# Kernel optimization log

Measured on AMD Instinct MI355X. Metric: run time of the kernel, lower is better.

The kernel has to match this reference:

```python
import jax, jax.numpy as jnp
import numpy as np

N_NODES = 100000
N_EDGES = 1600000
IN_CH, HID_CH, OUT_CH = 128, 128, 64


def _spmm(row, col, val, x, n):
    # COO sparse @ dense: out[r] += val_e * x[col_e]
    gathered = val[:, None] * x[col]  # [E, d]
    return jax.ops.segment_sum(gathered, row, num_segments=n)


def setup_inputs() -> dict:
    key = jax.random.key(0)
    ks = jax.random.split(key, 8)
    x = jax.random.normal(ks[0], (N_NODES, IN_CH), dtype=jnp.float32)
    adj_row = jax.random.randint(ks[1], (N_EDGES,), 0, N_NODES)
    adj_col = jax.random.randint(ks[2], (N_EDGES,), 0, N_NODES)
    adj_val = jax.random.uniform(ks[3], (N_EDGES,), dtype=jnp.float32)
    w1 = jax.random.normal(ks[4], (IN_CH, HID_CH), dtype=jnp.float32) * (1.0 / np.sqrt(IN_CH))
    b1 = jax.random.normal(ks[5], (HID_CH,), dtype=jnp.float32) * 0.01
    w2 = jax.random.normal(ks[6], (HID_CH, OUT_CH), dtype=jnp.float32) * (1.0 / np.sqrt(HID_CH))
    b2 = jax.random.normal(ks[7], (OUT_CH,), dtype=jnp.float32) * 0.01
    return {"x": x, "adj_row": adj_row, "adj_col": adj_col, "adj_val": adj_val,
            "w1": w1, "b1": b1, "w2": w2, "b2": b2}


def reference(x, adj_row, adj_col, adj_val, w1, b1, w2, b2):
    n = x.shape[0]
    # layer 1: spmm -> linear -> relu
    h = _spmm(adj_row, adj_col, adj_val, x, n)
    h = jax.nn.relu(h @ w1 + b1)
    # layer 2: spmm -> linear
    h = _spmm(adj_row, adj_col, adj_val, h, n)
    return h @ w2 + b2
```

## Files before the change

### kernel.cpp

```cpp
#include <hip/hip_runtime.h>


typedef __bf16 v8bf __attribute__((ext_vector_type(8)));
typedef float  v4f  __attribute__((ext_vector_type(4)));

#define MAXB 800

__device__ __forceinline__ unsigned short f2bf(float f) {
    unsigned u = __float_as_uint(f);
    unsigned r = u + 0x7fffu + ((u >> 16) & 1u);
    return (unsigned short)(r >> 16);
}

__global__ __launch_bounds__(256) void prep_k(const float* __restrict__ w1,
                                              const float* __restrict__ w2,
                                              unsigned short* __restrict__ w1T,
                                              unsigned short* __restrict__ w2T,
                                              int* __restrict__ counts,
                                              int* __restrict__ rowptr,
                                              int2* __restrict__ epkS, int E, int N) {
    int i = blockIdx.x * 256 + threadIdx.x;
    if (i < 16384) {
        int n = i >> 7, k = i & 127;
        w1T[i] = f2bf(w1[k * 128 + n]);
    } else if (i < 24576) {
        int i2 = i - 16384;
        int n = i2 >> 7, k = i2 & 127;
        w2T[i2] = f2bf(w2[k * 64 + n]);
    } else if (i < 24576 + MAXB) {
        counts[i - 24576] = 0;
    } else if (i < 24576 + MAXB + 32) {
        epkS[E + (i - 24576 - MAXB)] = make_int2(0, 0);
    } else if (i == 24576 + MAXB + 32) {
        rowptr[N] = E;
    }
}

__global__ __launch_bounds__(256) void hist_b(const int* __restrict__ arow,
                                              int* __restrict__ counts, int E, int B) {
    __shared__ int lh[MAXB];
    const int tid = threadIdx.x;
    for (int i = tid; i < B; i += 256) lh[i] = 0;
    __syncthreads();
    const int base = blockIdx.x * 4096;
#pragma unroll
    for (int j = 0; j < 16; ++j) {
        int i = base + j * 256 + tid;
        if (i < E) atomicAdd(&lh[arow[i] >> 7], 1);
    }
    __syncthreads();
    for (int i = tid; i < B; i += 256) {
        int c = lh[i];
        if (c) atomicAdd(&counts[i], c);
    }
}

__global__ __launch_bounds__(256) void scan_s(const int* __restrict__ counts,
                                              int* __restrict__ boff,
                                              int* __restrict__ gcursor, int B, int E) {
    __shared__ int lds[256];
    const int t = threadIdx.x;
    const int b0 = t * 4;
    int v[4];
    int s = 0;
#pragma unroll
    for (int j = 0; j < 4; ++j) {
        v[j] = (b0 + j < B) ? counts[b0 + j] : 0;
        s += v[j];
    }
    lds[t] = s;
    __syncthreads();
    for (int off = 1; off < 256; off <<= 1) {
        int tmp = 0;
        if (t >= off) tmp = lds[t - off];
        __syncthreads();
        if (t >= off) lds[t] += tmp;
        __syncthreads();
    }
    int run = (t > 0) ? lds[t - 1] : 0;
#pragma unroll
    for (int j = 0; j < 4; ++j) {
        if (b0 + j < B) {
            boff[b0 + j] = run;
            gcursor[b0 + j] = run;
        }
        run += v[j];
    }
    if (t == 255) boff[B] = E;
}

__global__ __launch_bounds__(256) void partition_k(const int* __restrict__ arow,
                                                   const int* __restrict__ acol,
                                                   const float* __restrict__ aval,
                                                   int* __restrict__ gcursor,
                                                   int2* __restrict__ epk, int E, int B) {
    __shared__ int2 ldata[4096];
    __shared__ int ldest[4096];
    __shared__ int lhist[MAXB];
    __shared__ int lscan[MAXB];
    __shared__ int ldelta[MAXB];
    __shared__ int lcur[MAXB];
    __shared__ int stmp[256];
    const int tid = threadIdx.x;
    const int base = blockIdx.x * 4096;
    const int cnt = min(4096, E - base);

    for (int i = tid; i < MAXB; i += 256) {
        lhist[i] = 0;
        lcur[i] = 0;
    }
    __syncthreads();

    int rr[16];
#pragma unroll
    for (int j = 0; j < 16; ++j) {
        int i = base + j * 256 + tid;
        rr[j] = (i < E) ? arow[i] : -1;
        if (rr[j] >= 0) atomicAdd(&lhist[rr[j] >> 7], 1);
    }
    __syncthreads();

    const int b0 = tid * 4;
    int v[4];
    int s = 0;
#pragma unroll
    for (int j = 0; j < 4; ++j) {
        v[j] = (b0 + j < MAXB) ? lhist[b0 + j] : 0;
        s += v[j];
    }
    stmp[tid] = s;
    __syncthreads();
    for (int off = 1; off < 256; off <<= 1) {
        int tmp = 0;
        if (tid >= off) tmp = stmp[tid - off];
        __syncthreads();
        if (tid >= off) stmp[tid] += tmp;
        __syncthreads();
    }
    int run = (tid > 0) ? stmp[tid - 1] : 0;
#pragma unroll
    for (int j = 0; j < 4; ++j) {
        if (b0 + j < MAXB) lscan[b0 + j] = run;
        run += v[j];
    }
    __syncthreads();

    for (int b = tid; b < B; b += 256) {
        int c = lhist[b];
        if (c) ldelta[b] = atomicAdd(&gcursor[b], c) - lscan[b];
    }
    __syncthreads();

#pragma unroll
    for (int j = 0; j < 16; ++j) {
        int i = base + j * 256 + tid;
        if (i < E) {
            int r = rr[j];
            int b = r >> 7;
            int lp = atomicAdd(&lcur[b], 1);
            int slot = lscan[b] + lp;
            int pk = acol[i] | ((r & 127) << 17);
            ldata[slot] = make_int2(pk, __float_as_int(aval[i]));
            ldest[slot] = ldelta[b] + slot;
        }
    }
    __syncthreads();

    for (int s2 = tid; s2 < cnt; s2 += 256) epk[ldest[s2]] = ldata[s2];
}

template <int NC, bool AF32>
__device__ __forceinline__ void gemm_body(const void* __restrict__ A,
                                          const unsigned short* __restrict__ wT,
                                          unsigned short* __restrict__ y, int M,
                                          int bid, char* smem) {
    constexpr int KP = 136;
    constexpr int NT = NC / 16;
    unsigned short* wl = (unsigned short*)smem;
    const int tid = threadIdx.x;
    for (int idx = tid; idx < NC * 16; idx += 256) {
        int n = idx >> 4, kc = idx & 15;
        *(uint4*)&wl[n * KP + kc * 8] = *(const uint4*)&wT[n * 128 + kc * 8];
    }
    __syncthreads();

    const int wave = tid >> 6;
    const int lane = tid & 63;
    const int m = lane & 15;
    const int q = lane >> 4;
    const int rowbase = bid * 64 + wave * 16;
    const int rowc = min(rowbase + m, M - 1);

    v4f acc[NT] = {};
    union LU { uint4 qv; v8bf b; };

#pragma unroll
    for (int ks = 0; ks < 4; ++ks) {
        const int k0 = ks * 32 + q * 8;
        v8bf a;
        if (AF32) {
            const float* Ap = (const float*)A + (size_t)rowc * 128 + k0;
            float4 f0 = *(const float4*)Ap;
            float4 f1 = *(const float4*)(Ap + 4);
            union { unsigned short s[8]; v8bf b; } cv;
            cv.s[0] = f2bf(f0.x); cv.s[1] = f2bf(f0.y);
            cv.s[2] = f2bf(f0.z); cv.s[3] = f2bf(f0.w);
            cv.s[4] = f2bf(f1.x); cv.s[5] = f2bf(f1.y);
            cv.s[6] = f2bf(f1.z); cv.s[7] = f2bf(f1.w);
            a = cv.b;
        } else {
            LU lu;
            lu.qv = *(const uint4*)((const unsigned short*)A + (size_t)rowc * 128 + k0);
            a = lu.b;
        }
#pragma unroll
        for (int nt = 0; nt < NT; ++nt) {
            v8bf b = *(const v8bf*)&wl[(nt * 16 + m) * KP + k0];
            acc[nt] = __builtin_amdgcn_mfma_f32_16x16x32_bf16(a, b, acc[nt], 0, 0, 0);
        }
    }
#pragma unroll
    for (int nt = 0; nt < NT; ++nt) {
#pragma unroll
        for (int r = 0; r < 4; ++r) {
            int orow = rowbase + q * 4 + r;
            if (orow < M) y[(size_t)orow * NC + nt * 16 + m] = f2bf(acc[nt][r]);
        }
    }
}

__global__ __launch_bounds__(256) void sort_gemm1(const int* __restrict__ boff,
                                                  const int2* __restrict__ epk,
                                                  int2* __restrict__ epkS,
                                                  int* __restrict__ rowptr, int N, int B,
                                                  const float* __restrict__ x,
                                                  const unsigned short* __restrict__ w1T,
                                                  unsigned short* __restrict__ y1b) {
    __shared__ __align__(16) char smem[34816];
    const int tid = threadIdx.x;
    if (blockIdx.x >= B) {
        gemm_body<128, true>(x, w1T, y1b, N, blockIdx.x - B, smem);
        return;
    }
    int2* sorted = (int2*)smem;
    int*  sc     = (int*)(smem + 32768);
    int*  lcur   = (int*)(smem + 32768 + 512);
    const int b = blockIdx.x;
    const int s = boff[b], e = boff[b + 1];
    const int cnt = min(e - s, 4096);
    if (tid < 128) sc[tid] = 0;
    __syncthreads();
    for (int i = s + tid; i < e; i += 256) {
        int rl = (epk[i].x >> 17) & 127;
        atomicAdd(&sc[rl], 1);
    }
    __syncthreads();
    int hv = (tid < 128) ? sc[tid] : 0;
    for (int off = 1; off < 128; off <<= 1) {
        int add = 0;
        if (tid < 128 && tid >= off) add = sc[tid - off];
        __syncthreads();
        if (tid < 128 && tid >= off) sc[tid] += add;
        __syncthreads();
    }
    if (tid < 128) {
        int ex = sc[tid] - hv;
        lcur[tid] = ex;
        int r = b * 128 + tid;
        if (r < N) rowptr[r] = s + ex;
    }
    __syncthreads();
    for (int i = s + tid; i < e; i += 256) {
        int2 p = epk[i];
        int rl = (p.x >> 17) & 127;
        int slot = atomicAdd(&lcur[rl], 1);
        if (slot < 4096) sorted[slot] = make_int2(p.x & 0x1FFFF, p.y);
    }
    __syncthreads();
    for (int i = tid; i < cnt; i += 256) epkS[s + i] = sorted[i];
}

__global__ __launch_bounds__(256) void gemm2_k(const unsigned short* __restrict__ h1b,
                                               const unsigned short* __restrict__ w2T,
                                               unsigned short* __restrict__ y2b, int M) {
    __shared__ __align__(16) char smem[64 * 136 * 2];
    gemm_body<64, false>(h1b, w2T, y2b, M, blockIdx.x, smem);
}

__global__ __launch_bounds__(256) void spmm128(const int* __restrict__ rowptr,
                                               const int2* __restrict__ ep,
                                               const unsigned short* __restrict__ yb,
                                               const float* __restrict__ bias,
                                               unsigned* __restrict__ outp, int N) {
    const int row = (blockIdx.x * 256 + threadIdx.x) >> 6;
    const int lane = threadIdx.x & 63;
    if (row >= N) return;
    const int s = rowptr[row], e = rowptr[row + 1];
    const unsigned* y32 = (const unsigned*)yb;
    float accx = 0.f, accy = 0.f;
    int2 cur[8];
#pragma unroll
    for (int k = 0; k < 8; ++k) cur[k] = ep[s + k];
    for (int j = s; j < e; j += 8) {
        int2 nxt[8];
#pragma unroll
        for (int k = 0; k < 8; ++k) nxt[k] = ep[j + 8 + k];
#pragma unroll
        for (int k = 0; k < 8; ++k) {
            float v = (j + k < e) ? __int_as_float(cur[k].y) : 0.f;
            unsigned u = y32[(size_t)cur[k].x * 64 + lane];
            accx += v * __uint_as_float(u << 16);
            accy += v * __uint_as_float(u & 0xffff0000u);
        }
#pragma unroll
        for (int k = 0; k < 8; ++k) cur[k] = nxt[k];
    }
    float2 bv = ((const float2*)bias)[lane];
    accx += bv.x;
    accy += bv.y;
    accx = fmaxf(accx, 0.f);
    accy = fmaxf(accy, 0.f);
    outp[(size_t)row * 64 + lane] = ((unsigned)f2bf(accy) << 16) | f2bf(accx);
}

__global__ __launch_bounds__(256) void spmm64(const int* __restrict__ rowptr,
                                              const int2* __restrict__ ep,
                                              const unsigned short* __restrict__ yb,
                                              const float* __restrict__ bias,
                                              float2* __restrict__ outp, int N) {
    const int row = (blockIdx.x * 256 + threadIdx.x) >> 6;
    const int lane = threadIdx.x & 63;
    if (row >= N) return;
    const int half = lane >> 5;
    const int sl = lane & 31;
    const int s = rowptr[row], e = rowptr[row + 1];
    const unsigned* y32 = (const unsigned*)yb;
    float accx = 0.f, accy = 0.f;
    int2 cur[8];
#pragma unroll
    for (int k = 0; k < 8; ++k) cur[k] = ep[s + 2 * k + half];
    for (int j = s; j < e; j += 16) {
        int2 nxt[8];
#pragma unroll
        for (int k = 0; k < 8; ++k) nxt[k] = ep[j + 16 + 2 * k + half];
#pragma unroll
        for (int k = 0; k < 8; ++k) {
            float v = (j + 2 * k + half < e) ? __int_as_float(cur[k].y) : 0.f;
            unsigned u = y32[(size_t)cur[k].x * 32 + sl];
            accx += v * __uint_as_float(u << 16);
            accy += v * __uint_as_float(u & 0xffff0000u);
        }
#pragma unroll
        for (int k = 0; k < 8; ++k) cur[k] = nxt[k];
    }
    accx += __shfl_xor(accx, 32, 64);
    accy += __shfl_xor(accy, 32, 64);
    if (sl == lane) {
        float2 bv = ((const float2*)bias)[sl];
        float2 o;
        o.x = accx + bv.x;
        o.y = accy + bv.y;
        outp[(size_t)row * 32 + sl] = o;
    }
}

extern "C" void kernel_launch(void* const* d_in, const int* in_sizes, int n_in,
                              void* d_out, int out_size, void* d_ws, size_t ws_size,
                              hipStream_t stream) {
    const float* x    = (const float*)d_in[0];
    const int*   arow = (const int*)d_in[1];
    const int*   acol = (const int*)d_in[2];
    const float* aval = (const float*)d_in[3];
    const float* w1   = (const float*)d_in[4];
    const float* b1   = (const float*)d_in[5];
    const float* w2   = (const float*)d_in[6];
    const float* b2   = (const float*)d_in[7];
    float*       out  = (float*)d_out;

    const int N = in_sizes[0] / 128;
    const int E = in_sizes[1];
    const int B = (N + 127) >> 7;

    char* p = (char*)d_ws;
    auto alloc = [&](size_t bytes) {
        char* r = p;
        p += (bytes + 255) & ~(size_t)255;
        return r;
    };
    int*            counts  = (int*)alloc((size_t)MAXB * 4);
    int*            boff    = (int*)alloc((size_t)(MAXB + 1) * 4);
    int*            gcursor = (int*)alloc((size_t)MAXB * 4);
    int*            rowptr  = (int*)alloc((size_t)(N + 1) * 4);
    int2*           epkS    = (int2*)alloc((size_t)(E + 32) * 8);
    unsigned short* w1T     = (unsigned short*)alloc(128 * 128 * 2);
    unsigned short* w2T     = (unsigned short*)alloc(64 * 128 * 2);
    unsigned short* y1b     = (unsigned short*)alloc((size_t)N * 128 * 2);
    unsigned short* h1b     = (unsigned short*)alloc((size_t)N * 128 * 2);
    unsigned short* y2b     = (unsigned short*)alloc((size_t)N * 64 * 2);
    int2*           epk     = (int2*)h1b;

    const int gemm_blocks = (N + 63) / 64;
    const int pb = (E + 4095) / 4096;

    prep_k<<<(24576 + MAXB + 33 + 255) / 256, 256, 0, stream>>>(
        w1, w2, w1T, w2T, counts, rowptr, epkS, E, N);
    hist_b<<<pb, 256, 0, stream>>>(arow, counts, E, B);
    scan_s<<<1, 256, 0, stream>>>(counts, boff, gcursor, B, E);
    partition_k<<<pb, 256, 0, stream>>>(arow, acol, aval, gcursor, epk, E, B);
    sort_gemm1<<<B + gemm_blocks, 256, 0, stream>>>(boff, epk, epkS, rowptr, N, B,
                                                    x, w1T, y1b);
    const int spmm_blocks = (N + 3) / 4;
    spmm128<<<spmm_blocks, 256, 0, stream>>>(rowptr, epkS, y1b, b1, (unsigned*)h1b, N);
    gemm2_k<<<gemm_blocks, 256, 0, stream>>>(h1b, w2T, y2b, N);
    spmm64<<<spmm_blocks, 256, 0, stream>>>(rowptr, epkS, y2b, b2, (float2*)out, N);
}
```

Before: 321.4 us.

## Fuse layer-1 SpMM with GEMM2 and merge weight prep into histogram

Layer-1 SpMM now writes each block's 64 rows of ReLU output into shared memory, and the same block immediately multiplies them by W2 with MFMA. This drops the h1 round trip through global memory and one launch. Weight conversion and padding are folded into the histogram kernel, and the counts buffer is zeroed with a memset. The final SpMM is rewritten so each lane handles one bf16 column with a 64-wide gather. Each wave now processes 16 rows serially in the fused kernel, which reduces parallelism and latency hiding for the gather. The edge-partition buffer now gets its own allocation instead of aliasing h1.

After: 313.7 us. -2.4%, faster.

```diff
diff --git a/kernel.cpp b/kernel.cpp
--- a/kernel.cpp
+++ b/kernel.cpp
@@ -12,34 +12,29 @@
     return (unsigned short)(r >> 16);
 }
 
-__global__ __launch_bounds__(256) void prep_k(const float* __restrict__ w1,
-                                              const float* __restrict__ w2,
-                                              unsigned short* __restrict__ w1T,
-                                              unsigned short* __restrict__ w2T,
-                                              int* __restrict__ counts,
-                                              int* __restrict__ rowptr,
-                                              int2* __restrict__ epkS, int E, int N) {
-    int i = blockIdx.x * 256 + threadIdx.x;
-    if (i < 16384) {
-        int n = i >> 7, k = i & 127;
-        w1T[i] = f2bf(w1[k * 128 + n]);
-    } else if (i < 24576) {
-        int i2 = i - 16384;
+__global__ __launch_bounds__(256) void hist_prep(const int* __restrict__ arow,
+                                                 int* __restrict__ counts, int E, int B,
+                                                 const float* __restrict__ w1,
+                                                 const float* __restrict__ w2,
+                                                 unsigned short* __restrict__ w1T,
+                                                 unsigned short* __restrict__ w2T,
+                                                 int* __restrict__ rowptr,
+                                                 int2* __restrict__ epkS, int N) {
+    const int tid = threadIdx.x;
+    int gi = blockIdx.x * 256 + tid;
+    if (gi < 16384) {
+        int n = gi >> 7, k = gi & 127;
+        w1T[gi] = f2bf(w1[k * 128 + n]);
+    } else if (gi < 24576) {
+        int i2 = gi - 16384;
         int n = i2 >> 7, k = i2 & 127;
         w2T[i2] = f2bf(w2[k * 64 + n]);
-    } else if (i < 24576 + MAXB) {
-        counts[i - 24576] = 0;
-    } else if (i < 24576 + MAXB + 32) {
-        epkS[E + (i - 24576 - MAXB)] = make_int2(0, 0);
-    } else if (i == 24576 + MAXB + 32) {
+    } else if (gi < 24576 + 32) {
+        epkS[E + (gi - 24576)] = make_int2(0, 0);
+    } else if (gi == 24576 + 32) {
         rowptr[N] = E;
     }
-}
-
-__global__ __launch_bounds__(256) void hist_b(const int* __restrict__ arow,
-                                              int* __restrict__ counts, int E, int B) {
     __shared__ int lh[MAXB];
-    const int tid = threadIdx.x;
     for (int i = tid; i < B; i += 256) lh[i] = 0;
     __syncthreads();
     const int base = blockIdx.x * 4096;
@@ -280,24 +275,82 @@
     for (int i = tid; i < cnt; i += 256) epkS[s + i] = sorted[i];
 }
 
-__global__ __launch_bounds__(256) void gemm2_k(const unsigned short* __restrict__ h1b,
-                                               const unsigned short* __restrict__ w2T,
-                                               unsigned short* __restrict__ y2b, int M) {
-    __shared__ __align__(16) char smem[64 * 136 * 2];
-    gemm_body<64, false>(h1b, w2T, y2b, M, blockIdx.x, smem);
-}
-
-__global__ __launch_bounds__(256) void spmm128(const int* __restrict__ rowptr,
-                                               const int2* __restrict__ ep,
-                                               const unsigned short* __restrict__ yb,
-                                               const float* __restrict__ bias,
-                                               unsigned* __restrict__ outp, int N) {
+__global__ __launch_bounds__(256) void spmm_gemm2(const int* __restrict__ rowptr,
+                                                  const int2* __restrict__ ep,
+                                                  const unsigned short* __restrict__ y1b,
+                                                  const float* __restrict__ b1,
+                                                  const unsigned short* __restrict__ w2T,
+                                                  unsigned short* __restrict__ y2b, int N) {
+    constexpr int KP = 136;
+    __shared__ unsigned short h1[64 * KP];
+    const int tid = threadIdx.x;
+    const int wave = tid >> 6, lane = tid & 63;
+    const int rowbase = blockIdx.x * 64;
+    const unsigned* y32 = (const unsigned*)y1b;
+    const float2 bv = ((const float2*)b1)[lane];
+
+    for (int i = 0; i < 16; ++i) {
+        const int r = rowbase + wave * 16 + i;
+        float accx = 0.f, accy = 0.f;
+        if (r < N) {
+            const int s = rowptr[r], e = rowptr[r + 1];
+            int2 cur[8];
+#pragma unroll
+            for (int k = 0; k < 8; ++k) cur[k] = ep[s + k];
+            for (int j = s; j < e; j += 8) {
+                int2 nxt[8];
+#pragma unroll
+                for (int k = 0; k < 8; ++k) nxt[k] = ep[j + 8 + k];
+#pragma unroll
+                for (int k = 0; k < 8; ++k) {
+                    float v = (j + k < e) ? __int_as_float(cur[k].y) : 0.f;
+                    unsigned u = y32[(size_t)cur[k].x * 64 + lane];
+                    accx += v * __uint_as_float(u << 16);
+                    accy += v * __uint_as_float(u & 0xffff0000u);
+                }
+#pragma unroll
+                for (int k = 0; k < 8; ++k) cur[k] = nxt[k];
+            }
+        }
+        accx = fmaxf(accx + bv.x, 0.f);
+        accy = fmaxf(accy + bv.y, 0.f);
+        unsigned pk = ((unsigned)f2bf(accy) << 16) | f2bf(accx);
+        *(unsigned*)&h1[(wave * 16 + i) * KP + 2 * lane] = pk;
+    }
+    __syncthreads();
+
+    const int m = lane & 15, q = lane >> 4;
+    v4f acc[4] = {};
+#pragma unroll
+    for (int ks = 0; ks < 4; ++ks) {
+        const int k0 = ks * 32 + q * 8;
+        v8bf a = *(const v8bf*)&h1[(wave * 16 + m) * KP + k0];
+#pragma unroll
+        for (int nt = 0; nt < 4; ++nt) {
+            v8bf b = *(const v8bf*)&w2T[(nt * 16 + m) * 128 + k0];
+            acc[nt] = __builtin_amdgcn_mfma_f32_16x16x32_bf16(a, b, acc[nt], 0, 0, 0);
+        }
+    }
+#pragma unroll
+    for (int nt = 0; nt < 4; ++nt) {
+#pragma unroll
+        for (int r = 0; r < 4; ++r) {
+            int orow = rowbase + wave * 16 + q * 4 + r;
+            if (orow < N) y2b[(size_t)orow * 64 + nt * 16 + m] = f2bf(acc[nt][r]);
+        }
+    }
+}
+
+__global__ __launch_bounds__(256) void spmm64(const int* __restrict__ rowptr,
+                                              const int2* __restrict__ ep,
+                                              const unsigned short* __restrict__ yb,
+                                              const float* __restrict__ bias,
+                                              float* __restrict__ outp, int N) {
     const int row = (blockIdx.x * 256 + threadIdx.x) >> 6;
     const int lane = threadIdx.x & 63;
     if (row >= N) return;
     const int s = rowptr[row], e = rowptr[row + 1];
-    const unsigned* y32 = (const unsigned*)yb;
-    float accx = 0.f, accy = 0.f;
+    float acc = 0.f;
     int2 cur[8];
 #pragma unroll
     for (int k = 0; k < 8; ++k) cur[k] = ep[s + k];
@@ -308,60 +361,14 @@
 #pragma unroll
         for (int k = 0; k < 8; ++k) {
             float v = (j + k < e) ? __int_as_float(cur[k].y) : 0.f;
-            unsigned u = y32[(size_t)cur[k].x * 64 + lane];
-            accx += v * __uint_as_float(u << 16);
-            accy += v * __uint_as_float(u & 0xffff0000u);
+            unsigned u = yb[(size_t)cur[k].x * 64 + lane];
+            acc += v * __uint_as_float(u << 16);
         }
 #pragma unroll
         for (int k = 0; k < 8; ++k) cur[k] = nxt[k];
     }
-    float2 bv = ((const float2*)bias)[lane];
-    accx += bv.x;
-    accy += bv.y;
-    accx = fmaxf(accx, 0.f);
-    accy = fmaxf(accy, 0.f);
-    outp[(size_t)row * 64 + lane] = ((unsigned)f2bf(accy) << 16) | f2bf(accx);
-}
-
-__global__ __launch_bounds__(256) void spmm64(const int* __restrict__ rowptr,
-                                              const int2* __restrict__ ep,
-                                              const unsigned short* __restrict__ yb,
-                                              const float* __restrict__ bias,
-                                              float2* __restrict__ outp, int N) {
-    const int row = (blockIdx.x * 256 + threadIdx.x) >> 6;
-    const int lane = threadIdx.x & 63;
-    if (row >= N) return;
-    const int half = lane >> 5;
-    const int sl = lane & 31;
-    const int s = rowptr[row], e = rowptr[row + 1];
-    const unsigned* y32 = (const unsigned*)yb;
-    float accx = 0.f, accy = 0.f;
-    int2 cur[8];
-#pragma unroll
-    for (int k = 0; k < 8; ++k) cur[k] = ep[s + 2 * k + half];
-    for (int j = s; j < e; j += 16) {
-        int2 nxt[8];
-#pragma unroll
-        for (int k = 0; k < 8; ++k) nxt[k] = ep[j + 16 + 2 * k + half];
-#pragma unroll
-        for (int k = 0; k < 8; ++k) {
-            float v = (j + 2 * k + half < e) ? __int_as_float(cur[k].y) : 0.f;
-            unsigned u = y32[(size_t)cur[k].x * 32 + sl];
-            accx += v * __uint_as_float(u << 16);
-            accy += v * __uint_as_float(u & 0xffff0000u);
-        }
-#pragma unroll
-        for (int k = 0; k < 8; ++k) cur[k] = nxt[k];
-    }
-    accx += __shfl_xor(accx, 32, 64);
-    accy += __shfl_xor(accy, 32, 64);
-    if (sl == lane) {
-        float2 bv = ((const float2*)bias)[sl];
-        float2 o;
-        o.x = accx + bv.x;
-        o.y = accy + bv.y;
-        outp[(size_t)row * 32 + sl] = o;
-    }
+    acc += bias[lane];
+    outp[(size_t)row * 64 + lane] = acc;
 }
 
 extern "C" void kernel_launch(void* const* d_in, const int* in_sizes, int n_in,
@@ -395,22 +402,20 @@
     unsigned short* w1T     = (unsigned short*)alloc(128 * 128 * 2);
     unsigned short* w2T     = (unsigned short*)alloc(64 * 128 * 2);
     unsigned short* y1b     = (unsigned short*)alloc((size_t)N * 128 * 2);
-    unsigned short* h1b     = (unsigned short*)alloc((size_t)N * 128 * 2);
+    int2*           epk     = (int2*)alloc((size_t)E * 8);
     unsigned short* y2b     = (unsigned short*)alloc((size_t)N * 64 * 2);
-    int2*           epk     = (int2*)h1b;
 
     const int gemm_blocks = (N + 63) / 64;
     const int pb = (E + 4095) / 4096;
 
-    prep_k<<<(24576 + MAXB + 33 + 255) / 256, 256, 0, stream>>>(
-        w1, w2, w1T, w2T, counts, rowptr, epkS, E, N);
-    hist_b<<<pb, 256, 0, stream>>>(arow, counts, E, B);
+    hipMemsetAsync(counts, 0, (size_t)MAXB * 4, stream);
+    hist_prep<<<pb, 256, 0, stream>>>(arow, counts, E, B, w1, w2, w1T, w2T,
+                                      rowptr, epkS, N);
     scan_s<<<1, 256, 0, stream>>>(counts, boff, gcursor, B, E);
     partition_k<<<pb, 256, 0, stream>>>(arow, acol, aval, gcursor, epk, E, B);
     sort_gemm1<<<B + gemm_blocks, 256, 0, stream>>>(boff, epk, epkS, rowptr, N, B,
                                                     x, w1T, y1b);
+    spmm_gemm2<<<gemm_blocks, 256, 0, stream>>>(rowptr, epkS, y1b, b1, w2T, y2b, N);
     const int spmm_blocks = (N + 3) / 4;
-    spmm128<<<spmm_blocks, 256, 0, stream>>>(rowptr, epkS, y1b, b1, (unsigned*)h1b, N);
-    gemm2_k<<<gemm_blocks, 256, 0, stream>>>(h1b, w2T, y2b, N);
-    spmm64<<<spmm_blocks, 256, 0, stream>>>(rowptr, epkS, y2b, b2, (float2*)out, N);
-}
+    spmm64<<<spmm_blocks, 256, 0, stream>>>(rowptr, epkS, y2b, b2, out, N);
+}
```
